# Kernel tuning notes

Measured on AMD Instinct MI355X. Metric: run time of the kernel, lower is better.

Reference implementation:

```python
import jax, jax.numpy as jnp
import numpy as np

B, S, E, H = 4, 2048, 512, 8
HD = E // H  # v head dim = 64; q/k per-head dim is E (=512) per the module's d_k


def setup_inputs() -> dict:
    key = jax.random.key(0)
    ks = jax.random.split(key, 4)
    def xav(k, shape):
        fan_in, fan_out = shape
        lim = float(np.sqrt(6.0 / (fan_in + fan_out)))
        return jax.random.uniform(k, shape, jnp.float32, -lim, lim)
    return {
        "x": jax.random.normal(ks[0], (B, S, E), jnp.float32),
        "Wqk": xav(ks[1], (E, 2 * E * H)),
        "bqk": jnp.zeros((2 * E * H,), jnp.float32),
        "Wv": xav(ks[2], (E, E)),
        "bv": jnp.zeros((E,), jnp.float32),
        "Wo": xav(ks[3], (E, E)),
        "bo": jnp.zeros((E,), jnp.float32),
    }


def reference(x, Wqk, bqk, Wv, bv, Wo, bo):
    # fused q/k projection: [B,S,E] @ [E, 2*E*H] -> [B,S,H,2E] -> [B,H,S,2E]
    qk = (x @ Wqk + bqk).reshape(B, S, H, 2 * E).transpose(0, 2, 1, 3)
    q, k = qk[..., :E], qk[..., E:]            # each [B,H,S,E]
    v = (x @ Wv + bv).reshape(B, S, H, HD).transpose(0, 2, 1, 3)  # [B,H,S,HD]
    scale = 1.0 / jnp.sqrt(jnp.asarray(E, x.dtype))
    scores = jnp.einsum("bhqe,bhke->bhqk", q, k) * scale
    attn = jax.nn.softmax(scores, axis=-1)
    vals = jnp.einsum("bhqk,bhkd->bhqd", attn, v)  # [B,H,S,HD]
    vals = vals.transpose(0, 2, 1, 3).reshape(B, S, E)
    return vals @ Wo + bo
```

## Files before the change

### kernel.cpp

```cpp
#include <hip/hip_runtime.h>
#include <cstdint>
#include <cstddef>

typedef unsigned short u16;
typedef unsigned char u8;
typedef long i64;
typedef __attribute__((ext_vector_type(8))) short bh8;
typedef __attribute__((ext_vector_type(4))) float fx4;
typedef __attribute__((ext_vector_type(8))) int i32x8;

__device__ __forceinline__ u16 f2bf(float f) {
  unsigned int u = __float_as_uint(f);
  u += 0x7fffu + ((u >> 16) & 1u);
  return (u16)(u >> 16);
}

__device__ __forceinline__ u8 f2e4m3(float f) {
  unsigned int u = __float_as_uint(f);
  unsigned int s = (u >> 24) & 0x80u;
  unsigned int mag = u & 0x7fffffffu;
  mag += 0x7ffffu + ((mag >> 20) & 1u);
  if (mag < 0x3C800000u) return (u8)s;
  unsigned int e8 = (mag >> 23) - 120u;
  unsigned int m8 = (mag >> 20) & 7u;
  return (u8)(s | (e8 << 3) | m8);
}

typedef __attribute__((address_space(1))) void g1_void;
typedef __attribute__((address_space(3))) void l3_void;
__device__ __forceinline__ void gload_lds16(const void* g, const void* lds) {
  __builtin_amdgcn_global_load_lds((g1_void*)(uintptr_t)g,
                                   (l3_void*)(unsigned int)(uintptr_t)lds,
                                   16, 0, 0);
}

__device__ __forceinline__ fx4 MFMA(bh8 a, bh8 b, fx4 c) {
  return __builtin_amdgcn_mfma_f32_16x16x32_bf16(a, b, c, 0, 0, 0);
}
__device__ __forceinline__ fx4 MFMAMX(i32x8 a, i32x8 b, fx4 c) {
  return __builtin_amdgcn_mfma_scale_f32_16x16x128_f8f6f4(a, b, c, 0, 0,
                                                          0, 0x7F, 0, 0x7F);
}
__device__ __forceinline__ i32x8 mk8(uint4 lo, uint4 hi) {
  i32x8 v;
  v[0] = (int)lo.x; v[1] = (int)lo.y; v[2] = (int)lo.z; v[3] = (int)lo.w;
  v[4] = (int)hi.x; v[5] = (int)hi.y; v[6] = (int)hi.z; v[7] = (int)hi.w;
  return v;
}

__global__ void prep(const float* __restrict__ x, u16* __restrict__ x_bf,
                     u8* __restrict__ x8,
                     const float* __restrict__ Wqk, u8* __restrict__ wqk8,
                     const float* __restrict__ Wv, u16* __restrict__ wvt,
                     const float* __restrict__ Wo, u16* __restrict__ wot) {
  __shared__ float t[32][33];
  const int bx = blockIdx.x;
  const int tx = threadIdx.x, ty = threadIdx.y;
  if (bx < 4096) {
    int i = bx * 256 + (ty * 32 + tx);
    float4 f = ((const float4*)x)[i];
    ushort4 u;
    u.x = f2bf(f.x); u.y = f2bf(f.y); u.z = f2bf(f.z); u.w = f2bf(f.w);
    ((ushort4*)x_bf)[i] = u;
    unsigned int p = (unsigned int)f2e4m3(f.x) | ((unsigned int)f2e4m3(f.y) << 8)
                   | ((unsigned int)f2e4m3(f.z) << 16) | ((unsigned int)f2e4m3(f.w) << 24);
    ((unsigned int*)x8)[i] = p;
  } else if (bx < 8192) {
    int b = bx - 4096;
    int c0 = (b & 255) * 32, r0 = (b >> 8) * 32;
#pragma unroll
    for (int i = 0; i < 4; i++)
      t[ty + i * 8][tx] = Wqk[(size_t)(r0 + ty + i * 8) * 8192 + c0 + tx];
    __syncthreads();
#pragma unroll
    for (int i = 0; i < 4; i++)
      wqk8[(size_t)(c0 + ty + i * 8) * 512 + r0 + tx] = f2e4m3(t[tx][ty + i * 8] * 256.0f);
  } else {
    int b = bx - 8192;
    const float* W = (b < 256) ? Wv : Wo;
    u16* Wt = (b < 256) ? wvt : wot;
    b &= 255;
    int c0 = (b & 15) * 32, r0 = (b >> 4) * 32;
#pragma unroll
    for (int i = 0; i < 4; i++)
      t[ty + i * 8][tx] = W[(size_t)(r0 + ty + i * 8) * 512 + c0 + tx];
    __syncthreads();
#pragma unroll
    for (int i = 0; i < 4; i++)
      Wt[(size_t)(c0 + ty + i * 8) * 512 + r0 + tx] = f2bf(t[tx][ty + i * 8]);
  }
}

__global__ __launch_bounds__(256) void gemm_qkv(
    const u8* __restrict__ A8, const u8* __restrict__ B8t,
    const float* __restrict__ bqk, u8* __restrict__ C8,
    const u16* __restrict__ A16, const u16* __restrict__ B16t,
    const float* __restrict__ bv, u16* __restrict__ vt) {
  __shared__ __align__(16) u8 smem[32768];
  const int tid = threadIdx.x;
  const int l = tid & 63, w = tid >> 6;
  const int lane15 = l & 15, quad = l >> 4;
  const int wm = (w >> 1) * 64, wn = (w & 1) * 64;
  const int bx = blockIdx.x;

  if (bx < 4096) {
    u8* As = smem;
    u8* Bs = smem + 16384;
    const int K = 512, N = 8192;
    const int bm = (bx >> 6) * 128, bn = (bx & 63) * 128;
    fx4 acc[4][4] = {};
    const int srow = w * 32 + (l >> 3);
    const int scol = ((l & 7) ^ ((l >> 3) & 7)) * 16;
    const u8* Ag = A8 + (size_t)(bm + srow) * K + scol;
    const u8* Bg = B8t + (size_t)(bn + srow) * K + scol;
    const int q2 = quad * 2;
    for (int kt = 0; kt < K; kt += 128) {
      __syncthreads();
#pragma unroll
      for (int c = 0; c < 4; c++) {
        gload_lds16(Ag + (size_t)(c * 8) * K + kt, As + (w * 32 + c * 8) * 128);
        gload_lds16(Bg + (size_t)(c * 8) * K + kt, Bs + (w * 32 + c * 8) * 128);
      }
      __syncthreads();
      i32x8 a[4], b[4];
#pragma unroll
      for (int mi = 0; mi < 4; mi++) {
        int r = wm + mi * 16 + lane15;
        const u8* rp = As + r * 128;
        a[mi] = mk8(*(const uint4*)(rp + ((q2 ^ (r & 7)) * 16)),
                    *(const uint4*)(rp + (((q2 + 1) ^ (r & 7)) * 16)));
      }
#pragma unroll
      for (int ni = 0; ni < 4; ni++) {
        int r = wn + ni * 16 + lane15;
        const u8* rp = Bs + r * 128;
        b[ni] = mk8(*(const uint4*)(rp + ((q2 ^ (r & 7)) * 16)),
                    *(const uint4*)(rp + (((q2 + 1) ^ (r & 7)) * 16)));
      }
#pragma unroll
      for (int mi = 0; mi < 4; mi++)
#pragma unroll
        for (int ni = 0; ni < 4; ni++)
          acc[mi][ni] = MFMAMX(a[mi], b[ni], acc[mi][ni]);
    }
#pragma unroll
    for (int mi = 0; mi < 4; mi++)
#pragma unroll
      for (int ni = 0; ni < 4; ni++) {
        int col = bn + wn + ni * 16 + lane15;
        float bvv = bqk[col];
#pragma unroll
        for (int r = 0; r < 4; r++) {
          int row = bm + wm + mi * 16 + quad * 4 + r;
          C8[(size_t)row * N + col] = f2e4m3(acc[mi][ni][r] * 0.00390625f + bvv);
        }
      }
  } else {
    u16* As = (u16*)smem;
    u16* Bs = (u16*)(smem + 16384);
    const int K = 512;
    const int b2 = bx - 4096;
    const int bm = (b2 >> 2) * 128, bn = (b2 & 3) * 128;
    fx4 acc[4][4] = {};
    const int srow = w * 32 + (l >> 3);
    const int scol = ((l & 7) ^ (l >> 3)) * 8;
    const u16* Ag = A16 + (size_t)(bm + srow) * K + scol;
    const u16* Bg = B16t + (size_t)(bn + srow) * K + scol;
    for (int kt = 0; kt < K; kt += 64) {
      __syncthreads();
#pragma unroll
      for (int c = 0; c < 4; c++) {
        gload_lds16(Ag + (size_t)(c * 8) * K + kt, As + (w * 32 + c * 8) * 64);
        gload_lds16(Bg + (size_t)(c * 8) * K + kt, Bs + (w * 32 + c * 8) * 64);
      }
      __syncthreads();
#pragma unroll
      for (int kk8 = 0; kk8 < 8; kk8 += 4) {
        bh8 a[4], b[4];
#pragma unroll
        for (int mi = 0; mi < 4; mi++) {
          int r = wm + mi * 16 + lane15;
          a[mi] = *(const bh8*)(As + r * 64 + (((kk8 + quad) ^ (r & 7)) * 8));
        }
#pragma unroll
        for (int ni = 0; ni < 4; ni++) {
          int r = wn + ni * 16 + lane15;
          b[ni] = *(const bh8*)(Bs + r * 64 + (((kk8 + quad) ^ (r & 7)) * 8));
        }
#pragma unroll
        for (int mi = 0; mi < 4; mi++)
#pragma unroll
          for (int ni = 0; ni < 4; ni++)
            acc[mi][ni] = MFMA(a[mi], b[ni], acc[mi][ni]);
      }
    }
#pragma unroll
    for (int mi = 0; mi < 4; mi++)
#pragma unroll
      for (int ni = 0; ni < 4; ni++) {
        int col = bn + wn + ni * 16 + lane15;
        float bvv = bv[col];
#pragma unroll
        for (int r = 0; r < 4; r++) {
          int row = bm + wm + mi * 16 + quad * 4 + r;
          float v = acc[mi][ni][r] + bvv;
          vt[((size_t)((row >> 11) * 512 + col) << 11) + (row & 2047)] = f2bf(v);
        }
      }
  }
}

__global__ __launch_bounds__(256) void gemm_bt(const u16* __restrict__ A,
                                               const u16* __restrict__ Bt,
                                               const float* __restrict__ bias,
                                               float* __restrict__ Cout,
                                               int M, int N, int K) {
  __shared__ u16 As[128 * 64];
  __shared__ u16 Bs[128 * 64];
  const int tid = threadIdx.x;
  const int l = tid & 63, w = tid >> 6;
  const int lane15 = l & 15, quad = l >> 4;
  const int wm = (w >> 1) * 64, wn = (w & 1) * 64;
  const int bm = blockIdx.y * 128, bn = blockIdx.x * 128;
  fx4 acc[4][4] = {};

  const int srow = w * 32 + (l >> 3);
  const int scol = ((l & 7) ^ (l >> 3)) * 8;
  const u16* Ag = A + (size_t)(bm + srow) * K + scol;
  const u16* Bg = Bt + (size_t)(bn + srow) * K + scol;

  for (int kt = 0; kt < K; kt += 64) {
    __syncthreads();
#pragma unroll
    for (int c = 0; c < 4; c++) {
      gload_lds16(Ag + (size_t)(c * 8) * K + kt, As + (w * 32 + c * 8) * 64);
      gload_lds16(Bg + (size_t)(c * 8) * K + kt, Bs + (w * 32 + c * 8) * 64);
    }
    __syncthreads();
#pragma unroll
    for (int kk8 = 0; kk8 < 8; kk8 += 4) {
      bh8 a[4], b[4];
#pragma unroll
      for (int mi = 0; mi < 4; mi++) {
        int r = wm + mi * 16 + lane15;
        a[mi] = *(const bh8*)(As + r * 64 + (((kk8 + quad) ^ (r & 7)) * 8));
      }
#pragma unroll
      for (int ni = 0; ni < 4; ni++) {
        int r = wn + ni * 16 + lane15;
        b[ni] = *(const bh8*)(Bs + r * 64 + (((kk8 + quad) ^ (r & 7)) * 8));
      }
#pragma unroll
      for (int mi = 0; mi < 4; mi++)
#pragma unroll
        for (int ni = 0; ni < 4; ni++)
          acc[mi][ni] = MFMA(a[mi], b[ni], acc[mi][ni]);
    }
  }
#pragma unroll
  for (int mi = 0; mi < 4; mi++)
#pragma unroll
    for (int ni = 0; ni < 4; ni++) {
      int col = bn + wn + ni * 16 + lane15;
      float bvv = bias[col];
#pragma unroll
      for (int r = 0; r < 4; r++) {
        int row = bm + wm + mi * 16 + quad * 4 + r;
        Cout[(size_t)row * N + col] = acc[mi][ni][r] + bvv;
      }
    }
}

__global__ __launch_bounds__(256, 2) void flash_attn(const u8* __restrict__ qk8,
                                                     const u16* __restrict__ vt,
                                                     u16* __restrict__ vals) {
  __shared__ __align__(16) u8 Ks[2][32 * 512];
  __shared__ __align__(16) u16 Vs[2][64 * 40];
  __shared__ __align__(16) u16 Ps[4][32 * 40];
  const int tid = threadIdx.x;
  const int l = tid & 63, w = tid >> 6;
  const int lane15 = l & 15, quad = l >> 4;
  const int q0 = blockIdx.x * 128;
  const int h = blockIdx.y, b = blockIdx.z;
  const float scale2 = 0.063762531f;
  const float Mb = 2.0f;

  i32x8 qmx[2][4];
#pragma unroll
  for (int mt = 0; mt < 2; mt++) {
    const u8* qrow = qk8 + (size_t)(b * 2048 + q0 + w * 32 + mt * 16 + lane15) * 8192
                   + h * 1024 + quad * 32;
#pragma unroll
    for (int e = 0; e < 4; e++)
      qmx[mt][e] = mk8(*(const uint4*)(qrow + e * 128),
                       *(const uint4*)(qrow + e * 128 + 16));
  }

  fx4 accO[2][4] = {};
  float lpart[2][4] = {};

  const u8* kbase = qk8 + (size_t)(b * 2048) * 8192 + h * 1024 + 512;
  const u16* vrow = vt + (size_t)((b * 8 + h) * 64 + (tid >> 2)) * 2048 + (tid & 3) * 8;
  const int vs_off = (tid >> 2) * 40 + (tid & 3) * 8;

  uint4 vreg = *(const uint4*)vrow;
#pragma unroll
  for (int c = 0; c < 4; c++) {
    int R0 = w * 8 + 2 * c;
    int r = R0 + (l >> 5);
    gload_lds16(kbase + (size_t)r * 8192 + (((l & 31) ^ (r & 7)) * 16),
                &Ks[0][R0 * 512]);
  }

  for (int t = 0; t < 64; t++) {
    const int cb = t & 1, nb = cb ^ 1;
    const int kt0 = t * 32;
    __syncthreads();

    bh8 pf0, pf1, vf0, vf1, vf2, vf3;
    if (t > 0) {
      const u16* vsb = &Vs[(t - 1) & 1][0];
      pf0 = *(const bh8*)(&Ps[w][lane15 * 40 + quad * 8]);
      pf1 = *(const bh8*)(&Ps[w][(16 + lane15) * 40 + quad * 8]);
      vf0 = *(const bh8*)(vsb + (lane15)      * 40 + quad * 8);
      vf1 = *(const bh8*)(vsb + (16 + lane15) * 40 + quad * 8);
      vf2 = *(const bh8*)(vsb + (32 + lane15) * 40 + quad * 8);
      vf3 = *(const bh8*)(vsb + (48 + lane15) * 40 + quad * 8);
    }

    *(uint4*)&Vs[cb][vs_off] = vreg;

    if (t < 63) {
#pragma unroll
      for (int c = 0; c < 4; c++) {
        int R0 = w * 8 + 2 * c;
        int r = R0 + (l >> 5);
        gload_lds16(kbase + (size_t)(kt0 + 32 + r) * 8192 + (((l & 31) ^ (r & 7)) * 16),
                    &Ks[nb][R0 * 512]);
      }
      vreg = *(const uint4*)(vrow + kt0 + 32);
    }

    if (t > 0) {
      accO[0][0] = MFMA(pf0, vf0, accO[0][0]); accO[1][0] = MFMA(pf1, vf0, accO[1][0]);
      accO[0][1] = MFMA(pf0, vf1, accO[0][1]); accO[1][1] = MFMA(pf1, vf1, accO[1][1]);
      accO[0][2] = MFMA(pf0, vf2, accO[0][2]); accO[1][2] = MFMA(pf1, vf2, accO[1][2]);
      accO[0][3] = MFMA(pf0, vf3, accO[0][3]); accO[1][3] = MFMA(pf1, vf3, accO[1][3]);
    }

    fx4 accS[2][2] = {};
    {
      const int xsw = lane15 & 7;
      const u8* rp0 = &Ks[cb][lane15 * 512];
      const u8* rp1 = &Ks[cb][(16 + lane15) * 512];
#pragma unroll
      for (int e = 0; e < 4; e++) {
        int c0 = e * 8 + quad * 2;
        i32x8 kb0 = mk8(*(const uint4*)(rp0 + ((c0 ^ xsw) * 16)),
                        *(const uint4*)(rp0 + (((c0 + 1) ^ xsw) * 16)));
        i32x8 kb1 = mk8(*(const uint4*)(rp1 + ((c0 ^ xsw) * 16)),
                        *(const uint4*)(rp1 + (((c0 + 1) ^ xsw) * 16)));
        accS[0][0] = MFMAMX(qmx[0][e], kb0, accS[0][0]);
        accS[1][0] = MFMAMX(qmx[1][e], kb0, accS[1][0]);
        accS[0][1] = MFMAMX(qmx[0][e], kb1, accS[0][1]);
        accS[1][1] = MFMAMX(qmx[1][e], kb1, accS[1][1]);
      }
    }

#pragma unroll
    for (int mt = 0; mt < 2; mt++)
#pragma unroll
      for (int r = 0; r < 4; r++) {
        float p0 = __builtin_amdgcn_exp2f(__fmaf_rn(accS[mt][0][r], scale2, -Mb));
        float p1 = __builtin_amdgcn_exp2f(__fmaf_rn(accS[mt][1][r], scale2, -Mb));
        lpart[mt][r] += p0 + p1;
        Ps[w][(mt * 16 + quad * 4 + r) * 40 + lane15]      = f2bf(p0);
        Ps[w][(mt * 16 + quad * 4 + r) * 40 + 16 + lane15] = f2bf(p1);
      }
  }

  {
    const u16* vsb = &Vs[1][0];
    bh8 pf0 = *(const bh8*)(&Ps[w][lane15 * 40 + quad * 8]);
    bh8 pf1 = *(const bh8*)(&Ps[w][(16 + lane15) * 40 + quad * 8]);
#pragma unroll
    for (int di = 0; di < 4; di++) {
      bh8 vf = *(const bh8*)(vsb + (di * 16 + lane15) * 40 + quad * 8);
      accO[0][di] = MFMA(pf0, vf, accO[0][di]);
      accO[1][di] = MFMA(pf1, vf, accO[1][di]);
    }
  }

#pragma unroll
  for (int mt = 0; mt < 2; mt++)
#pragma unroll
    for (int r = 0; r < 4; r++) {
      float s = lpart[mt][r];
      s += __shfl_xor(s, 1);
      s += __shfl_xor(s, 2);
      s += __shfl_xor(s, 4);
      s += __shfl_xor(s, 8);
      float inv = 1.0f / s;
      int row = q0 + w * 32 + mt * 16 + quad * 4 + r;
      u16* orow = vals + (size_t)(b * 2048 + row) * 512 + h * 64 + lane15;
#pragma unroll
      for (int di = 0; di < 4; di++) orow[di * 16] = f2bf(accO[mt][di][r] * inv);
    }
}

extern "C" void kernel_launch(void* const* d_in, const int* in_sizes, int n_in,
                              void* d_out, int out_size, void* d_ws, size_t ws_size,
                              hipStream_t stream) {
  const float* x   = (const float*)d_in[0];
  const float* Wqk = (const float*)d_in[1];
  const float* bqk = (const float*)d_in[2];
  const float* Wv  = (const float*)d_in[3];
  const float* bv  = (const float*)d_in[4];
  const float* Wo  = (const float*)d_in[5];
  const float* bo  = (const float*)d_in[6];
  float* out = (float*)d_out;

  char* ws = (char*)d_ws;
  u16* x_bf  = (u16*)(ws);
  u8*  x8    = (u8*)(ws + 8388608);
  u8*  wqk8  = (u8*)(ws + 12582912);
  u16* wvt   = (u16*)(ws + 16777216);
  u16* wot   = (u16*)(ws + 17301504);
  u16* vtbuf = (u16*)(ws + 17825792);
  u16* valsb = (u16*)(ws + 26214400);
  u8*  qk8   = (u8*)(ws + 34603008);

  prep<<<8704, dim3(32, 8), 0, stream>>>(x, x_bf, x8, Wqk, wqk8, Wv, wvt, Wo, wot);

  gemm_qkv<<<4352, 256, 0, stream>>>(x8, wqk8, bqk, qk8, x_bf, wvt, bv, vtbuf);

  flash_attn<<<dim3(16, 8, 4), 256, 0, stream>>>(qk8, vtbuf, valsb);

  gemm_bt<<<dim3(4, 64), 256, 0, stream>>>(valsb, wot, bo, out, 8192, 512, 512);
}
```

Measured before the change: 268.2 us.

## Software-pipeline flash attention: overlap softmax of previous tile with QK MFMA

After: 262.7 us. 2.0% less time.

```diff
diff --git a/kernel.cpp b/kernel.cpp
--- a/kernel.cpp
+++ b/kernel.cpp
@@ -271,12 +271,83 @@
     }
 }
 
+#define FLASH_BODY(T, CUR, PREV)                                              \
+  {                                                                           \
+    const int t_ = (T);                                                       \
+    const int cb = t_ & 1, nb = cb ^ 1;                                       \
+    const int kt0 = t_ * 32;                                                  \
+    __syncthreads();                             \
+    bh8 pf0, pf1, vf0, vf1, vf2, vf3;                                         \
+    if (t_ > 1) {                                       \
+      const u16* vsb = &Vs[(t_ + 1) % 3][0];                  \
+      const u16* psb = &Ps[cb][w][0];                         \
+      pf0 = *(const bh8*)(psb + lane15 * 40 + quad * 8);                      \
+      pf1 = *(const bh8*)(psb + (16 + lane15) * 40 + quad * 8);               \
+      vf0 = *(const bh8*)(vsb + (lane15)*40 + quad * 8);                      \
+      vf1 = *(const bh8*)(vsb + (16 + lane15) * 40 + quad * 8);               \
+      vf2 = *(const bh8*)(vsb + (32 + lane15) * 40 + quad * 8);               \
+      vf3 = *(const bh8*)(vsb + (48 + lane15) * 40 + quad * 8);               \
+    }                                                                         \
+    *(uint4*)&Vs[t_ % 3][vs_off] = vreg;                      \
+    if (t_ < 63) {                             \
+      _Pragma("unroll")                                                       \
+      for (int c = 0; c < 4; c++) {                                           \
+        int R0 = w * 8 + 2 * c;                                               \
+        int r = R0 + (l >> 5);                                                \
+        gload_lds16(kbase + (size_t)(kt0 + 32 + r) * 8192 +                   \
+                        (((l & 31) ^ (r & 7)) * 16),                          \
+                    &Ks[nb][R0 * 512]);                                       \
+      }                                                                       \
+      vreg = *(const uint4*)(vrow + kt0 + 32);                    \
+    }                                                                         \
+    if (t_ > 1) {                                          \
+      accO[0][0] = MFMA(pf0, vf0, accO[0][0]);                                \
+      accO[1][0] = MFMA(pf1, vf0, accO[1][0]);                                \
+      accO[0][1] = MFMA(pf0, vf1, accO[0][1]);                                \
+      accO[1][1] = MFMA(pf1, vf1, accO[1][1]);                                \
+      accO[0][2] = MFMA(pf0, vf2, accO[0][2]);                                \
+      accO[1][2] = MFMA(pf1, vf2, accO[1][2]);                                \
+      accO[0][3] = MFMA(pf0, vf3, accO[0][3]);                                \
+      accO[1][3] = MFMA(pf1, vf3, accO[1][3]);                                \
+    }                                                                         \
+    if (t_ > 0) {                           \
+      u16* ps = &Ps[nb][w][0];                                                \
+      _Pragma("unroll")                                                       \
+      for (int mt = 0; mt < 2; mt++)                                          \
+        _Pragma("unroll")                                                     \
+        for (int r = 0; r < 4; r++) {                                         \
+          float p0 = __builtin_amdgcn_exp2f(__fmaf_rn(PREV[mt][0][r], scale2, -Mb)); \
+          float p1 = __builtin_amdgcn_exp2f(__fmaf_rn(PREV[mt][1][r], scale2, -Mb)); \
+          lpart[mt][r] += p0 + p1;                                            \
+          ps[(mt * 16 + quad * 4 + r) * 40 + lane15]      = f2bf(p0);         \
+          ps[(mt * 16 + quad * 4 + r) * 40 + 16 + lane15] = f2bf(p1);         \
+        }                                                                     \
+    }                                                                         \
+    {                                              \
+      const u8* rp0 = &Ks[cb][lane15 * 512];                                  \
+      const u8* rp1 = &Ks[cb][(16 + lane15) * 512];                           \
+      CUR[0][0] = fz; CUR[0][1] = fz; CUR[1][0] = fz; CUR[1][1] = fz;         \
+      _Pragma("unroll")                                                       \
+      for (int e = 0; e < 4; e++) {                                           \
+        int c0 = e * 8 + quad * 2;                                            \
+        i32x8 kb0 = mk8(*(const uint4*)(rp0 + ((c0 ^ xsw) * 16)),             \
+                        *(const uint4*)(rp0 + (((c0 + 1) ^ xsw) * 16)));      \
+        i32x8 kb1 = mk8(*(const uint4*)(rp1 + ((c0 ^ xsw) * 16)),             \
+                        *(const uint4*)(rp1 + (((c0 + 1) ^ xsw) * 16)));      \
+        CUR[0][0] = MFMAMX(qmx[0][e], kb0, CUR[0][0]);                        \
+        CUR[1][0] = MFMAMX(qmx[1][e], kb0, CUR[1][0]);                        \
+        CUR[0][1] = MFMAMX(qmx[0][e], kb1, CUR[0][1]);                        \
+        CUR[1][1] = MFMAMX(qmx[1][e], kb1, CUR[1][1]);                        \
+      }                                                                       \
+    }                                                                         \
+  }
+
 __global__ __launch_bounds__(256, 2) void flash_attn(const u8* __restrict__ qk8,
                                                      const u16* __restrict__ vt,
                                                      u16* __restrict__ vals) {
   __shared__ __align__(16) u8 Ks[2][32 * 512];
-  __shared__ __align__(16) u16 Vs[2][64 * 40];
-  __shared__ __align__(16) u16 Ps[4][32 * 40];
+  __shared__ __align__(16) u16 Vs[3][64 * 40];
+  __shared__ __align__(16) u16 Ps[2][4][32 * 40];
   const int tid = threadIdx.x;
   const int l = tid & 63, w = tid >> 6;
   const int lane15 = l & 15, quad = l >> 4;
@@ -284,6 +355,8 @@
   const int h = blockIdx.y, b = blockIdx.z;
   const float scale2 = 0.063762531f;
   const float Mb = 2.0f;
+  const fx4 fz = {};
+  const int xsw = lane15 & 7;
 
   i32x8 qmx[2][4];
 #pragma unroll
@@ -298,6 +371,7 @@
 
   fx4 accO[2][4] = {};
   float lpart[2][4] = {};
+  fx4 aSa[2][2] = {}, aSb[2][2] = {};
 
   const u8* kbase = qk8 + (size_t)(b * 2048) * 8192 + h * 1024 + 512;
   const u16* vrow = vt + (size_t)((b * 8 + h) * 64 + (tid >> 2)) * 2048 + (tid & 3) * 8;
@@ -312,77 +386,42 @@
                 &Ks[0][R0 * 512]);
   }
 
-  for (int t = 0; t < 64; t++) {
-    const int cb = t & 1, nb = cb ^ 1;
-    const int kt0 = t * 32;
-    __syncthreads();
-
-    bh8 pf0, pf1, vf0, vf1, vf2, vf3;
-    if (t > 0) {
-      const u16* vsb = &Vs[(t - 1) & 1][0];
-      pf0 = *(const bh8*)(&Ps[w][lane15 * 40 + quad * 8]);
-      pf1 = *(const bh8*)(&Ps[w][(16 + lane15) * 40 + quad * 8]);
-      vf0 = *(const bh8*)(vsb + (lane15)      * 40 + quad * 8);
-      vf1 = *(const bh8*)(vsb + (16 + lane15) * 40 + quad * 8);
-      vf2 = *(const bh8*)(vsb + (32 + lane15) * 40 + quad * 8);
-      vf3 = *(const bh8*)(vsb + (48 + lane15) * 40 + quad * 8);
-    }
-
-    *(uint4*)&Vs[cb][vs_off] = vreg;
-
-    if (t < 63) {
-#pragma unroll
-      for (int c = 0; c < 4; c++) {
-        int R0 = w * 8 + 2 * c;
-        int r = R0 + (l >> 5);
-        gload_lds16(kbase + (size_t)(kt0 + 32 + r) * 8192 + (((l & 31) ^ (r & 7)) * 16),
-                    &Ks[nb][R0 * 512]);
-      }
-      vreg = *(const uint4*)(vrow + kt0 + 32);
-    }
-
-    if (t > 0) {
-      accO[0][0] = MFMA(pf0, vf0, accO[0][0]); accO[1][0] = MFMA(pf1, vf0, accO[1][0]);
-      accO[0][1] = MFMA(pf0, vf1, accO[0][1]); accO[1][1] = MFMA(pf1, vf1, accO[1][1]);
-      accO[0][2] = MFMA(pf0, vf2, accO[0][2]); accO[1][2] = MFMA(pf1, vf2, accO[1][2]);
-      accO[0][3] = MFMA(pf0, vf3, accO[0][3]); accO[1][3] = MFMA(pf1, vf3, accO[1][3]);
-    }
-
-    fx4 accS[2][2] = {};
-    {
-      const int xsw = lane15 & 7;
-      const u8* rp0 = &Ks[cb][lane15 * 512];
-      const u8* rp1 = &Ks[cb][(16 + lane15) * 512];
-#pragma unroll
-      for (int e = 0; e < 4; e++) {
-        int c0 = e * 8 + quad * 2;
-        i32x8 kb0 = mk8(*(const uint4*)(rp0 + ((c0 ^ xsw) * 16)),
-                        *(const uint4*)(rp0 + (((c0 + 1) ^ xsw) * 16)));
-        i32x8 kb1 = mk8(*(const uint4*)(rp1 + ((c0 ^ xsw) * 16)),
-                        *(const uint4*)(rp1 + (((c0 + 1) ^ xsw) * 16)));
-        accS[0][0] = MFMAMX(qmx[0][e], kb0, accS[0][0]);
-        accS[1][0] = MFMAMX(qmx[1][e], kb0, accS[1][0]);
-        accS[0][1] = MFMAMX(qmx[0][e], kb1, accS[0][1]);
-        accS[1][1] = MFMAMX(qmx[1][e], kb1, accS[1][1]);
-      }
-    }
-
+  for (int tt = 0; tt < 32; tt++) {
+    FLASH_BODY(2 * tt,     aSa, aSb);
+    FLASH_BODY(2 * tt + 1, aSb, aSa);
+  }
+
+  {
+    u16* ps = &Ps[1][w][0];
 #pragma unroll
     for (int mt = 0; mt < 2; mt++)
 #pragma unroll
       for (int r = 0; r < 4; r++) {
-        float p0 = __builtin_amdgcn_exp2f(__fmaf_rn(accS[mt][0][r], scale2, -Mb));
-        float p1 = __builtin_amdgcn_exp2f(__fmaf_rn(accS[mt][1][r], scale2, -Mb));
+        float p0 = __builtin_amdgcn_exp2f(__fmaf_rn(aSb[mt][0][r], scale2, -Mb));
+        float p1 = __builtin_amdgcn_exp2f(__fmaf_rn(aSb[mt][1][r], scale2, -Mb));
         lpart[mt][r] += p0 + p1;
-        Ps[w][(mt * 16 + quad * 4 + r) * 40 + lane15]      = f2bf(p0);
-        Ps[w][(mt * 16 + quad * 4 + r) * 40 + 16 + lane15] = f2bf(p1);
-      }
-  }
-
+        ps[(mt * 16 + quad * 4 + r) * 40 + lane15]      = f2bf(p0);
+        ps[(mt * 16 + quad * 4 + r) * 40 + 16 + lane15] = f2bf(p1);
+      }
+  }
   {
-    const u16* vsb = &Vs[1][0];
-    bh8 pf0 = *(const bh8*)(&Ps[w][lane15 * 40 + quad * 8]);
-    bh8 pf1 = *(const bh8*)(&Ps[w][(16 + lane15) * 40 + quad * 8]);
+    const u16* vsb = &Vs[2][0];
+    const u16* psb = &Ps[0][w][0];
+    bh8 pf0 = *(const bh8*)(psb + lane15 * 40 + quad * 8);
+    bh8 pf1 = *(const bh8*)(psb + (16 + lane15) * 40 + quad * 8);
+#pragma unroll
+    for (int di = 0; di < 4; di++) {
+      bh8 vf = *(const bh8*)(vsb + (di * 16 + lane15) * 40 + quad * 8);
+      accO[0][di] = MFMA(pf0, vf, accO[0][di]);
+      accO[1][di] = MFMA(pf1, vf, accO[1][di]);
+    }
+  }
+  __syncthreads();
+  {
+    const u16* vsb = &Vs[0][0];
+    const u16* psb = &Ps[1][w][0];
+    bh8 pf0 = *(const bh8*)(psb + lane15 * 40 + quad * 8);
+    bh8 pf1 = *(const bh8*)(psb + (16 + lane15) * 40 + quad * 8);
 #pragma unroll
     for (int di = 0; di < 4; di++) {
       bh8 vf = *(const bh8*)(vsb + (di * 16 + lane15) * 40 + quad * 8);
```
